# Performance work log

Hardware: AMD Instinct MI355X
Metric: run time of the kernel (lower is better)

## Reference

```python
import jax, jax.numpy as jnp
import numpy as np

N = 50000
E = 800000
FEAT = 512
HID = 256
CLS = 40
EPS = 1e-5


def setup_inputs() -> dict:
    key = jax.random.key(0)
    ks = jax.random.split(key, 8)
    x = jax.random.normal(ks[0], (N, FEAT), dtype=jnp.float32)
    edge_index = jax.random.randint(ks[1], (2, E), 0, N, dtype=jnp.int64)
    s = 0.05
    return {
        "x": x,
        "edge_index": edge_index,
        "W1": jax.random.normal(ks[2], (FEAT, HID), dtype=jnp.float32) * s,
        "b1": jnp.zeros((HID,), jnp.float32),
        "W2": jax.random.normal(ks[3], (HID, HID), dtype=jnp.float32) * s,
        "b2": jnp.zeros((HID,), jnp.float32),
        "W3": jax.random.normal(ks[4], (HID, CLS), dtype=jnp.float32) * s,
        "b3": jnp.zeros((CLS,), jnp.float32),
        "gamma": jnp.ones((HID,), jnp.float32),
        "beta": jnp.zeros((HID,), jnp.float32),
        "run_mean": jnp.zeros((HID,), jnp.float32),
        "run_var": jnp.ones((HID,), jnp.float32),
    }


def _edge_norm(edge_index):
    # add self-loops, then symmetric normalization D^-1/2 (A+I) D^-1/2
    loop = jnp.arange(N, dtype=edge_index.dtype)
    src = jnp.concatenate([edge_index[0], loop])
    dst = jnp.concatenate([edge_index[1], loop])
    deg = jax.ops.segment_sum(jnp.ones_like(dst, jnp.float32), dst, num_segments=N)
    inv_sqrt = jnp.where(deg > 0, jax.lax.rsqrt(jnp.maximum(deg, 1.0)), 0.0)
    norm = inv_sqrt[src] * inv_sqrt[dst]  # [E+N]
    return src, dst, norm


def _gcn_conv(x, W, b, src, dst, norm):
    h = x @ W                               # [N, out]
    msg = h[src] * norm[:, None]            # gather + scale, [E+N, out]
    out = jax.ops.segment_sum(msg, dst, num_segments=N)
    return out + b


def _bn_relu(x, gamma, beta, mean, var):
    return jax.nn.relu((x - mean) * jax.lax.rsqrt(var + EPS) * gamma + beta)


def reference(x, edge_index, W1, b1, W2, b2, W3, b3, gamma, beta, run_mean, run_var):
    src, dst, norm = _edge_norm(edge_index)
    h = _gcn_conv(x, W1, b1, src, dst, norm)
    h = _bn_relu(h, gamma, beta, run_mean, run_var)
    h = _gcn_conv(h, W2, b2, src, dst, norm)
    h = _bn_relu(h, gamma, beta, run_mean, run_var)
    h = _gcn_conv(h, W3, b3, src, dst, norm)
    return h
```

## Files before the change

kernel.cpp:

```cpp
#include <hip/hip_runtime.h>
#include <cstdint>
#include <cstddef>

#define FEAT 512
#define HID 256
#define CLS 40
#define EPS 1e-5f

typedef __attribute__((ext_vector_type(8))) short short8;
typedef __attribute__((ext_vector_type(4))) float f32x4v;


__device__ __forceinline__ unsigned short f2bf(float f) {
    union { float f; unsigned u; } v; v.f = f;
    unsigned r = v.u + 0x7FFF + ((v.u >> 16) & 1);
    return (unsigned short)(r >> 16);
}
__device__ __forceinline__ float bf2f(unsigned short h) {
    union { unsigned u; float f; } v; v.u = ((unsigned)h) << 16;
    return v.f;
}

typedef const __attribute__((address_space(1))) unsigned int* gas_ptr;
typedef __attribute__((address_space(3))) unsigned int* las_ptr;
__device__ __forceinline__ void lds_load16(const void* g, void* l) {
    __builtin_amdgcn_global_load_lds((gas_ptr)g, (las_ptr)l, 16, 0, 0);
}

__device__ __forceinline__ float4 f4add(float4 a, float4 b) {
    return make_float4(a.x + b.x, a.y + b.y, a.z + b.z, a.w + b.w);
}

__device__ __forceinline__ void accum_bf4(float4& a, ushort4 v) {
    a.x += bf2f(v.x); a.y += bf2f(v.y); a.z += bf2f(v.z); a.w += bf2f(v.w);
}


__global__ __launch_bounds__(256) void prep_cvt_kernel(
        const float* __restrict__ x, const float* __restrict__ W1, const float* __restrict__ W2,
        int* __restrict__ counts, int* __restrict__ fillpos,
        unsigned short* __restrict__ w1hi, unsigned short* __restrict__ w1lo,
        unsigned short* __restrict__ w2hi, unsigned short* __restrict__ w2lo,
        unsigned short* __restrict__ xbf, int N) {
    int i = blockIdx.x * 256 + threadIdx.x;
    const int n0 = N;
    const int n1 = FEAT * HID;
    const int n2 = HID * HID;
    const int n3 = N * FEAT / 8;
    if (i < n0) { counts[i] = 0; fillpos[i] = 0; return; }
    i -= n0;
    if (i < n1) {
        int k = i / HID, n = i % HID;
        float f = W1[i];
        unsigned short h = f2bf(f);
        w1hi[(size_t)n * FEAT + k] = h;
        w1lo[(size_t)n * FEAT + k] = f2bf(f - bf2f(h));
        return;
    }
    i -= n1;
    if (i < n2) {
        int k = i / HID, n = i % HID;
        float f = W2[i];
        unsigned short h = f2bf(f);
        w2hi[(size_t)n * HID + k] = h;
        w2lo[(size_t)n * HID + k] = f2bf(f - bf2f(h));
        return;
    }
    i -= n2;
    if (i < n3) {
        const float4* xp = (const float4*)x;
        float4 a = xp[2 * i], b = xp[2 * i + 1];
        float f[8] = {a.x, a.y, a.z, a.w, b.x, b.y, b.z, b.w};
        short8 h;
#pragma unroll
        for (int j = 0; j < 8; ++j) h[j] = (short)f2bf(f[j]);
        ((short8*)xbf)[i] = h;
    }
}


__global__ void hist_kernel(const int* __restrict__ dst, int* __restrict__ counts, int E) {
    int e = blockIdx.x * 256 + threadIdx.x;
    if (e < E) atomicAdd(&counts[dst[e]], 1);
}

__global__ void scan_block_kernel(const int* __restrict__ counts, int* __restrict__ row_ptr,
                                  int* __restrict__ blocksums, int n) {
    __shared__ int s[256];
    int tid = threadIdx.x;
    int i = blockIdx.x * 256 + tid;
    int v = (i < n) ? counts[i] : 0;
    s[tid] = v; __syncthreads();
    for (int off = 1; off < 256; off <<= 1) {
        int t = (tid >= off) ? s[tid - off] : 0;
        __syncthreads();
        s[tid] += t;
        __syncthreads();
    }
    if (i < n) row_ptr[i] = s[tid] - v;
    if (tid == 255) blocksums[blockIdx.x] = s[255];
}

__global__ void finalize_rowptr_kernel(int* __restrict__ row_ptr, const int* __restrict__ blocksums,
                                       const int* __restrict__ counts, float* __restrict__ inv_sqrt,
                                       int n, int E, int nb) {
    __shared__ int s[256];
    __shared__ int excl[256];
    int tid = threadIdx.x;
    int v = (tid < nb) ? blocksums[tid] : 0;
    s[tid] = v; __syncthreads();
    for (int off = 1; off < 256; off <<= 1) {
        int t = (tid >= off) ? s[tid - off] : 0;
        __syncthreads();
        s[tid] += t;
        __syncthreads();
    }
    excl[tid] = s[tid] - v;
    __syncthreads();
    int i = blockIdx.x * 256 + tid;
    if (i < n) {
        row_ptr[i] += excl[i >> 8];
        inv_sqrt[i] = rsqrtf((float)(counts[i] + 1));
    }
    if (i == 0) row_ptr[n] = E;
}

__global__ void fill_kernel(const int* __restrict__ src, const int* __restrict__ dst,
                            const int* __restrict__ row_ptr, int* __restrict__ fillpos,
                            int* __restrict__ src_sorted, int E) {
    int e = blockIdx.x * 256 + threadIdx.x;
    if (e < E) {
        int d = dst[e];
        int pos = row_ptr[d] + atomicAdd(&fillpos[d], 1);
        src_sorted[pos] = src[e];
    }
}


template<int BK>
__global__ __launch_bounds__(256) void gemm_mfma_kernel(
        const unsigned short* __restrict__ gA,
        const unsigned short* __restrict__ Wthi, const unsigned short* __restrict__ Wtlo,
        const float* __restrict__ inv_sqrt, unsigned short* __restrict__ C,
        int M, int K, int Ncol) {
    constexpr int BLK = 16 * BK;
    constexpr int CH = BK / 32;
    __shared__ unsigned short AhiL[2][128 * BK];
    __shared__ unsigned short BhiL[2][128 * BK];
    __shared__ unsigned short BloL[2][128 * BK];
    const int tid  = threadIdx.x;
    const int lane = tid & 63;
    const int w    = tid >> 6;
    const int wr   = w >> 1, wc = w & 1;
    const int lm   = lane & 15;
    const int lk8  = (lane >> 4) * 8;
    const int bm   = blockIdx.x * 128;
    const int bn   = blockIdx.y * 128;

    f32x4v acc[4][4] = {};

    int nc0 = bn + 16 * (2 * w) + lm;
    int nc1 = bn + 16 * (2 * w + 1) + lm;
    const unsigned short* gB_h0 = Wthi + (size_t)nc0 * K + lk8;
    const unsigned short* gB_h1 = Wthi + (size_t)nc1 * K + lk8;
    const unsigned short* gB_l0 = Wtlo + (size_t)nc0 * K + lk8;
    const unsigned short* gB_l1 = Wtlo + (size_t)nc1 * K + lk8;

    int ar0 = bm + 16 * (2 * w) + lm;     if (ar0 >= M) ar0 = M - 1;
    int ar1 = bm + 16 * (2 * w + 1) + lm; if (ar1 >= M) ar1 = M - 1;
    const unsigned short* gA_h0 = gA + (size_t)ar0 * K + lk8;
    const unsigned short* gA_h1 = gA + (size_t)ar1 * K + lk8;

    auto stage = [&](int buf, int k0) {
#pragma unroll
        for (int kk = 0; kk < CH; ++kk) {
            const int kg = k0 + 32 * kk;
            const int lo = kk * 512;
            lds_load16(gA_h0 + kg, &AhiL[buf][(2 * w) * BLK + lo]);
            lds_load16(gA_h1 + kg, &AhiL[buf][(2 * w + 1) * BLK + lo]);
            lds_load16(gB_h0 + kg, &BhiL[buf][(2 * w) * BLK + lo]);
            lds_load16(gB_h1 + kg, &BhiL[buf][(2 * w + 1) * BLK + lo]);
            lds_load16(gB_l0 + kg, &BloL[buf][(2 * w) * BLK + lo]);
            lds_load16(gB_l1 + kg, &BloL[buf][(2 * w + 1) * BLK + lo]);
        }
    };

    auto compute = [&](int buf) {
#pragma unroll
        for (int half = 0; half < CH; ++half) {
            const int ho = half * 512;
            short8 ah[4], bh[4], bv[4];
#pragma unroll
            for (int i = 0; i < 4; ++i) {
                int ao = (wr * 4 + i) * BLK + ho + lane * 8;
                int bo = (wc * 4 + i) * BLK + ho + lane * 8;
                ah[i] = *(const short8*)&AhiL[buf][ao];
                bh[i] = *(const short8*)&BhiL[buf][bo];
                bv[i] = *(const short8*)&BloL[buf][bo];
            }
#pragma unroll
            for (int i = 0; i < 4; ++i)
#pragma unroll
                for (int j = 0; j < 4; ++j) {
                    acc[i][j] = __builtin_amdgcn_mfma_f32_16x16x32_bf16(ah[i], bh[j], acc[i][j], 0, 0, 0);
                    acc[i][j] = __builtin_amdgcn_mfma_f32_16x16x32_bf16(ah[i], bv[j], acc[i][j], 0, 0, 0);
                }
        }
    };

    stage(0, 0);
    __syncthreads();
    int cur = 0;
    for (int k0 = BK; k0 < K; k0 += BK) {
        stage(cur ^ 1, k0);
        compute(cur);
        __syncthreads();
        cur ^= 1;
    }
    compute(cur);

    const int orow_base = bm + wr * 64;
    const int ocol_base = bn + wc * 64 + lm;
    const int rq = (lane >> 4) * 4;
#pragma unroll
    for (int i = 0; i < 4; ++i) {
#pragma unroll
        for (int r = 0; r < 4; ++r) {
            int row = orow_base + i * 16 + rq + r;
            if (row >= M) continue;
            float s = inv_sqrt[row];
            size_t rb = (size_t)row * Ncol;
#pragma unroll
            for (int j = 0; j < 4; ++j)
                C[rb + ocol_base + j * 16] = f2bf(acc[i][j][r] * s);
        }
    }
}


__global__ __launch_bounds__(256) void gemm_scaled_hl_kernel(
        const unsigned short* __restrict__ Ahi, const unsigned short* __restrict__ Alo,
        const float* __restrict__ W,
        const float* __restrict__ inv_sqrt, float* __restrict__ C,
        int M, int K, int Ncol) {
    __shared__ float As[16][64];
    __shared__ float Ws[16][64];
    int tid = threadIdx.x;
    int tm = tid >> 4;
    int tn = tid & 15;
    int bm = blockIdx.x * 64;
    int bn = blockIdx.y * 64;

    float acc[4][4] = {};

    int lr = tid >> 2;
    int lc = (tid & 3) << 2;
    int wr = tid >> 4;
    int wc = (tid & 15) << 2;
    int arow = bm + lr;
    bool aok = arow < M;
    bool wok = (bn + wc) < Ncol;
    const unsigned short* AhiRow = Ahi + (size_t)arow * K + lc;
    const unsigned short* AloRow = Alo + (size_t)arow * K + lc;

    for (int k0 = 0; k0 < K; k0 += 16) {
        float4 av = make_float4(0.f, 0.f, 0.f, 0.f);
        if (aok) {
            ushort4 hv = *(const ushort4*)(AhiRow + k0);
            ushort4 lv = *(const ushort4*)(AloRow + k0);
            av.x = bf2f(hv.x) + bf2f(lv.x);
            av.y = bf2f(hv.y) + bf2f(lv.y);
            av.z = bf2f(hv.z) + bf2f(lv.z);
            av.w = bf2f(hv.w) + bf2f(lv.w);
        }
        As[lc + 0][lr] = av.x; As[lc + 1][lr] = av.y;
        As[lc + 2][lr] = av.z; As[lc + 3][lr] = av.w;

        float4 wv = make_float4(0.f, 0.f, 0.f, 0.f);
        if (wok) wv = *(const float4*)(W + (size_t)(k0 + wr) * Ncol + bn + wc);
        *(float4*)&Ws[wr][wc] = wv;
        __syncthreads();

#pragma unroll
        for (int k = 0; k < 16; ++k) {
            const float4 a4 = *(const float4*)&As[k][tm << 2];
            const float4 b4 = *(const float4*)&Ws[k][tn << 2];
            float a[4] = {a4.x, a4.y, a4.z, a4.w};
            float b[4] = {b4.x, b4.y, b4.z, b4.w};
#pragma unroll
            for (int i = 0; i < 4; ++i)
#pragma unroll
                for (int j = 0; j < 4; ++j)
                    acc[i][j] = fmaf(a[i], b[j], acc[i][j]);
        }
        __syncthreads();
    }

#pragma unroll
    for (int i = 0; i < 4; ++i) {
        int row = bm + (tm << 2) + i;
        if (row >= M) continue;
        float s = inv_sqrt[row];
        int col = bn + (tn << 2);
        if (col < Ncol) {
            float4 o = make_float4(acc[i][0] * s, acc[i][1] * s, acc[i][2] * s, acc[i][3] * s);
            *(float4*)&C[(size_t)row * Ncol + col] = o;
        }
    }
}


template<bool WRITE_LO>
__global__ __launch_bounds__(256) void agg_bn_hl_kernel(
        const unsigned short* __restrict__ g, const int* __restrict__ row_ptr,
        const int* __restrict__ srcs, const float* __restrict__ inv_sqrt,
        const float* __restrict__ bias, const float* __restrict__ gamma,
        const float* __restrict__ beta, const float* __restrict__ mean,
        const float* __restrict__ var,
        unsigned short* __restrict__ out_hi, unsigned short* __restrict__ out_lo, int n) {
    int node = (blockIdx.x << 2) + (threadIdx.x >> 6);
    int lane = threadIdx.x & 63;
    if (node >= n) return;
    const ushort4* gp = (const ushort4*)g;
    float4 acc0 = make_float4(0.f, 0.f, 0.f, 0.f);
    float4 acc1 = make_float4(0.f, 0.f, 0.f, 0.f);
    accum_bf4(acc0, gp[(size_t)node * 64 + lane]);
    int beg = row_ptr[node];
    int cnt = row_ptr[node + 1] - beg;

    for (int base = 0; base < cnt; base += 64) {
        int m = cnt - base; if (m > 64) m = 64;
        int idx = (lane < m) ? srcs[beg + base + lane] : 0;
        int j = 0;
        for (; j + 8 <= m; j += 8) {
            int s0 = __shfl(idx, j + 0), s1 = __shfl(idx, j + 1);
            int s2 = __shfl(idx, j + 2), s3 = __shfl(idx, j + 3);
            int s4 = __shfl(idx, j + 4), s5 = __shfl(idx, j + 5);
            int s6 = __shfl(idx, j + 6), s7 = __shfl(idx, j + 7);
            ushort4 v0 = gp[(size_t)s0 * 64 + lane];
            ushort4 v1 = gp[(size_t)s1 * 64 + lane];
            ushort4 v2 = gp[(size_t)s2 * 64 + lane];
            ushort4 v3 = gp[(size_t)s3 * 64 + lane];
            ushort4 v4 = gp[(size_t)s4 * 64 + lane];
            ushort4 v5 = gp[(size_t)s5 * 64 + lane];
            ushort4 v6 = gp[(size_t)s6 * 64 + lane];
            ushort4 v7 = gp[(size_t)s7 * 64 + lane];
            accum_bf4(acc0, v0); accum_bf4(acc0, v1);
            accum_bf4(acc0, v2); accum_bf4(acc0, v3);
            accum_bf4(acc1, v4); accum_bf4(acc1, v5);
            accum_bf4(acc1, v6); accum_bf4(acc1, v7);
        }
        for (; j < m; ++j) {
            int s = __shfl(idx, j);
            accum_bf4(acc0, gp[(size_t)s * 64 + lane]);
        }
    }
    float4 acc = f4add(acc0, acc1);

    float inv = inv_sqrt[node];
    float4 b4  = ((const float4*)bias)[lane];
    float4 ga4 = ((const float4*)gamma)[lane];
    float4 be4 = ((const float4*)beta)[lane];
    float4 m4  = ((const float4*)mean)[lane];
    float4 v4  = ((const float4*)var)[lane];
    float4 o;
    o.x = fmaxf((acc.x * inv + b4.x - m4.x) * (ga4.x * rsqrtf(v4.x + EPS)) + be4.x, 0.f);
    o.y = fmaxf((acc.y * inv + b4.y - m4.y) * (ga4.y * rsqrtf(v4.y + EPS)) + be4.y, 0.f);
    o.z = fmaxf((acc.z * inv + b4.z - m4.z) * (ga4.z * rsqrtf(v4.z + EPS)) + be4.z, 0.f);
    o.w = fmaxf((acc.w * inv + b4.w - m4.w) * (ga4.w * rsqrtf(v4.w + EPS)) + be4.w, 0.f);
    ushort4 oh;
    oh.x = f2bf(o.x); oh.y = f2bf(o.y); oh.z = f2bf(o.z); oh.w = f2bf(o.w);
    ((ushort4*)out_hi)[(size_t)node * 64 + lane] = oh;
    if (WRITE_LO) {
        ushort4 ol;
        ol.x = f2bf(o.x - bf2f(oh.x));
        ol.y = f2bf(o.y - bf2f(oh.y));
        ol.z = f2bf(o.z - bf2f(oh.z));
        ol.w = f2bf(o.w - bf2f(oh.w));
        ((ushort4*)out_lo)[(size_t)node * 64 + lane] = ol;
    }
}


__global__ __launch_bounds__(256) void agg_final_kernel(
        const float* __restrict__ g, const int* __restrict__ row_ptr,
        const int* __restrict__ srcs, const float* __restrict__ inv_sqrt,
        const float* __restrict__ bias, float* __restrict__ out, int n) {
    int node = (blockIdx.x << 2) + (threadIdx.x >> 6);
    int lane = threadIdx.x & 63;
    if (node >= n) return;
    int flane = (lane < CLS) ? lane : 0;
    float acc0 = g[(size_t)node * CLS + flane];
    float acc1 = 0.f;
    int beg = row_ptr[node];
    int cnt = row_ptr[node + 1] - beg;

    for (int base = 0; base < cnt; base += 64) {
        int m = cnt - base; if (m > 64) m = 64;
        int idx = (lane < m) ? srcs[beg + base + lane] : 0;
        int j = 0;
        for (; j + 8 <= m; j += 8) {
            int s0 = __shfl(idx, j + 0), s1 = __shfl(idx, j + 1);
            int s2 = __shfl(idx, j + 2), s3 = __shfl(idx, j + 3);
            int s4 = __shfl(idx, j + 4), s5 = __shfl(idx, j + 5);
            int s6 = __shfl(idx, j + 6), s7 = __shfl(idx, j + 7);
            float v0 = g[(size_t)s0 * CLS + flane];
            float v1 = g[(size_t)s1 * CLS + flane];
            float v2 = g[(size_t)s2 * CLS + flane];
            float v3 = g[(size_t)s3 * CLS + flane];
            float v4 = g[(size_t)s4 * CLS + flane];
            float v5 = g[(size_t)s5 * CLS + flane];
            float v6 = g[(size_t)s6 * CLS + flane];
            float v7 = g[(size_t)s7 * CLS + flane];
            acc0 += (v0 + v1) + (v2 + v3);
            acc1 += (v4 + v5) + (v6 + v7);
        }
        for (; j < m; ++j) {
            int s = __shfl(idx, j);
            acc0 += g[(size_t)s * CLS + flane];
        }
    }
    if (lane < CLS)
        out[(size_t)node * CLS + lane] = (acc0 + acc1) * inv_sqrt[node] + bias[lane];
}


extern "C" void kernel_launch(void* const* d_in, const int* in_sizes, int n_in,
                              void* d_out, int out_size, void* d_ws, size_t ws_size,
                              hipStream_t stream) {
    const float* x     = (const float*)d_in[0];
    const int*   edges = (const int*)d_in[1];
    const float* W1    = (const float*)d_in[2];
    const float* b1    = (const float*)d_in[3];
    const float* W2    = (const float*)d_in[4];
    const float* b2    = (const float*)d_in[5];
    const float* W3    = (const float*)d_in[6];
    const float* b3    = (const float*)d_in[7];
    const float* gamma = (const float*)d_in[8];
    const float* beta  = (const float*)d_in[9];
    const float* mean  = (const float*)d_in[10];
    const float* var   = (const float*)d_in[11];

    const int N = in_sizes[0] / FEAT;
    const int E = in_sizes[1] / 2;
    const int* src = edges;
    const int* dst = edges + E;

    char* ws = (char*)d_ws;
    auto alloc = [&](size_t bytes) -> char* {
        char* p = ws;
        ws += (bytes + 255) & ~(size_t)255;
        return p;
    };
    int*   counts     = (int*)  alloc((size_t)N * 4);
    int*   fillpos    = (int*)  alloc((size_t)N * 4);
    int*   row_ptr    = (int*)  alloc((size_t)(N + 1) * 4);
    int*   blocksums  = (int*)  alloc(256 * 4);
    float* inv_sqrt   = (float*)alloc((size_t)N * 4);
    int*   src_sorted = (int*)  alloc((size_t)E * 4);
    unsigned short* w1hi = (unsigned short*)alloc((size_t)FEAT * HID * 2);
    unsigned short* w1lo = (unsigned short*)alloc((size_t)FEAT * HID * 2);
    unsigned short* w2hi = (unsigned short*)alloc((size_t)HID * HID * 2);
    unsigned short* w2lo = (unsigned short*)alloc((size_t)HID * HID * 2);
    unsigned short* g    = (unsigned short*)alloc((size_t)N * HID * 2);
    unsigned short* h_hi = (unsigned short*)alloc((size_t)N * HID * 2);
    unsigned short* h_lo = (unsigned short*)alloc((size_t)N * HID * 2);
    unsigned short* xbf  = h_hi;

    int nb = (N + 255) / 256;
    int eb = (E + 255) / 256;

    int prep_items = N + FEAT * HID + HID * HID + N * FEAT / 8;
    prep_cvt_kernel<<<(prep_items + 255) / 256, 256, 0, stream>>>(
        x, W1, W2, counts, fillpos, w1hi, w1lo, w2hi, w2lo, xbf, N);
    hist_kernel<<<eb, 256, 0, stream>>>(dst, counts, E);
    scan_block_kernel<<<nb, 256, 0, stream>>>(counts, row_ptr, blocksums, N);
    finalize_rowptr_kernel<<<nb, 256, 0, stream>>>(row_ptr, blocksums, counts, inv_sqrt, N, E, nb);
    fill_kernel<<<eb, 256, 0, stream>>>(src, dst, row_ptr, fillpos, src_sorted, E);

    dim3 mfma_grid((N + 127) / 128, HID / 128);
    dim3 gemm3_grid((N + 63) / 64, 1);
    dim3 agg_grid((N + 3) / 4);

    gemm_mfma_kernel<32><<<mfma_grid, 256, 0, stream>>>(
        xbf, w1hi, w1lo, inv_sqrt, g, N, FEAT, HID);
    agg_bn_hl_kernel<false><<<agg_grid, 256, 0, stream>>>(g, row_ptr, src_sorted, inv_sqrt,
                                                          b1, gamma, beta, mean, var, h_hi, nullptr, N);
    gemm_mfma_kernel<32><<<mfma_grid, 256, 0, stream>>>(
        h_hi, w2hi, w2lo, inv_sqrt, g, N, HID, HID);
    agg_bn_hl_kernel<true><<<agg_grid, 256, 0, stream>>>(g, row_ptr, src_sorted, inv_sqrt,
                                                         b2, gamma, beta, mean, var, h_hi, h_lo, N);
    float* g3 = (float*)g;
    gemm_scaled_hl_kernel<<<gemm3_grid, 256, 0, stream>>>(h_hi, h_lo, W3, inv_sqrt, g3, N, HID, CLS);
    agg_final_kernel<<<agg_grid, 256, 0, stream>>>(g3, row_ptr, src_sorted, inv_sqrt,
                                                   b3, (float*)d_out, N);
}
```

Measured before the change: 548.1 us.

## Load GEMM MFMA fragments directly from global into registers, bypassing LDS

Replaces the LDS double-buffered global_load_lds staging in the MFMA GEMM with direct per-lane global loads into register fragments. A register double buffer is software-pipelined over a compile-time K loop. This removes LDS traffic and block barriers. In exchange, A and B fragments are no longer shared across waves through LDS, so each wave issues redundant global and L2 loads, and register pressure rises.

```diff
diff --git a/kernel.cpp b/kernel.cpp
--- a/kernel.cpp
+++ b/kernel.cpp
@@ -19,12 +19,6 @@
 __device__ __forceinline__ float bf2f(unsigned short h) {
     union { unsigned u; float f; } v; v.u = ((unsigned)h) << 16;
     return v.f;
-}
-
-typedef const __attribute__((address_space(1))) unsigned int* gas_ptr;
-typedef __attribute__((address_space(3))) unsigned int* las_ptr;
-__device__ __forceinline__ void lds_load16(const void* g, void* l) {
-    __builtin_amdgcn_global_load_lds((gas_ptr)g, (las_ptr)l, 16, 0, 0);
 }
 
 __device__ __forceinline__ float4 f4add(float4 a, float4 b) {
@@ -137,17 +131,29 @@
 }
 
 
-template<int BK>
-__global__ __launch_bounds__(256) void gemm_mfma_kernel(
+#define LOADF(A, B, V, k0)                                    \
+    _Pragma("unroll")                                         \
+    for (int i = 0; i < 4; ++i) {                             \
+        A[i] = *(const short8*)(pa[i] + (k0));                \
+        B[i] = *(const short8*)(pbh[i] + (k0));               \
+        V[i] = *(const short8*)(pbv[i] + (k0));               \
+    }
+
+#define COMPF(A, B, V)                                        \
+    _Pragma("unroll")                                         \
+    for (int i = 0; i < 4; ++i)                               \
+        _Pragma("unroll")                                     \
+        for (int j = 0; j < 4; ++j) {                         \
+            acc[i][j] = __builtin_amdgcn_mfma_f32_16x16x32_bf16(A[i], B[j], acc[i][j], 0, 0, 0); \
+            acc[i][j] = __builtin_amdgcn_mfma_f32_16x16x32_bf16(A[i], V[j], acc[i][j], 0, 0, 0); \
+        }
+
+template<int K>
+__global__ __launch_bounds__(256) void gemm_mfma_direct_kernel(
         const unsigned short* __restrict__ gA,
         const unsigned short* __restrict__ Wthi, const unsigned short* __restrict__ Wtlo,
         const float* __restrict__ inv_sqrt, unsigned short* __restrict__ C,
-        int M, int K, int Ncol) {
-    constexpr int BLK = 16 * BK;
-    constexpr int CH = BK / 32;
-    __shared__ unsigned short AhiL[2][128 * BK];
-    __shared__ unsigned short BhiL[2][128 * BK];
-    __shared__ unsigned short BloL[2][128 * BK];
+        int M, int Ncol) {
     const int tid  = threadIdx.x;
     const int lane = tid & 63;
     const int w    = tid >> 6;
@@ -159,65 +165,32 @@
 
     f32x4v acc[4][4] = {};
 
-    int nc0 = bn + 16 * (2 * w) + lm;
-    int nc1 = bn + 16 * (2 * w + 1) + lm;
-    const unsigned short* gB_h0 = Wthi + (size_t)nc0 * K + lk8;
-    const unsigned short* gB_h1 = Wthi + (size_t)nc1 * K + lk8;
-    const unsigned short* gB_l0 = Wtlo + (size_t)nc0 * K + lk8;
-    const unsigned short* gB_l1 = Wtlo + (size_t)nc1 * K + lk8;
-
-    int ar0 = bm + 16 * (2 * w) + lm;     if (ar0 >= M) ar0 = M - 1;
-    int ar1 = bm + 16 * (2 * w + 1) + lm; if (ar1 >= M) ar1 = M - 1;
-    const unsigned short* gA_h0 = gA + (size_t)ar0 * K + lk8;
-    const unsigned short* gA_h1 = gA + (size_t)ar1 * K + lk8;
-
-    auto stage = [&](int buf, int k0) {
-#pragma unroll
-        for (int kk = 0; kk < CH; ++kk) {
-            const int kg = k0 + 32 * kk;
-            const int lo = kk * 512;
-            lds_load16(gA_h0 + kg, &AhiL[buf][(2 * w) * BLK + lo]);
-            lds_load16(gA_h1 + kg, &AhiL[buf][(2 * w + 1) * BLK + lo]);
-            lds_load16(gB_h0 + kg, &BhiL[buf][(2 * w) * BLK + lo]);
-            lds_load16(gB_h1 + kg, &BhiL[buf][(2 * w + 1) * BLK + lo]);
-            lds_load16(gB_l0 + kg, &BloL[buf][(2 * w) * BLK + lo]);
-            lds_load16(gB_l1 + kg, &BloL[buf][(2 * w + 1) * BLK + lo]);
-        }
-    };
-
-    auto compute = [&](int buf) {
-#pragma unroll
-        for (int half = 0; half < CH; ++half) {
-            const int ho = half * 512;
-            short8 ah[4], bh[4], bv[4];
-#pragma unroll
-            for (int i = 0; i < 4; ++i) {
-                int ao = (wr * 4 + i) * BLK + ho + lane * 8;
-                int bo = (wc * 4 + i) * BLK + ho + lane * 8;
-                ah[i] = *(const short8*)&AhiL[buf][ao];
-                bh[i] = *(const short8*)&BhiL[buf][bo];
-                bv[i] = *(const short8*)&BloL[buf][bo];
-            }
-#pragma unroll
-            for (int i = 0; i < 4; ++i)
-#pragma unroll
-                for (int j = 0; j < 4; ++j) {
-                    acc[i][j] = __builtin_amdgcn_mfma_f32_16x16x32_bf16(ah[i], bh[j], acc[i][j], 0, 0, 0);
-                    acc[i][j] = __builtin_amdgcn_mfma_f32_16x16x32_bf16(ah[i], bv[j], acc[i][j], 0, 0, 0);
-                }
-        }
-    };
-
-    stage(0, 0);
-    __syncthreads();
-    int cur = 0;
-    for (int k0 = BK; k0 < K; k0 += BK) {
-        stage(cur ^ 1, k0);
-        compute(cur);
-        __syncthreads();
-        cur ^= 1;
-    }
-    compute(cur);
+    const unsigned short* pa[4];
+    const unsigned short* pbh[4];
+    const unsigned short* pbv[4];
+#pragma unroll
+    for (int i = 0; i < 4; ++i) {
+        int ar = bm + wr * 64 + i * 16 + lm; if (ar >= M) ar = M - 1;
+        pa[i]  = gA   + (size_t)ar * K + lk8;
+        int nc = bn + wc * 64 + i * 16 + lm;
+        pbh[i] = Wthi + (size_t)nc * K + lk8;
+        pbv[i] = Wtlo + (size_t)nc * K + lk8;
+    }
+
+    short8 a0[4], b0[4], v0[4], a1[4], b1[4], v1[4];
+
+    LOADF(a0, b0, v0, 0);
+    int k0 = 0;
+#pragma unroll
+    for (; k0 + 64 < K; k0 += 64) {
+        LOADF(a1, b1, v1, k0 + 32);
+        COMPF(a0, b0, v0);
+        LOADF(a0, b0, v0, k0 + 64);
+        COMPF(a1, b1, v1);
+    }
+    LOADF(a1, b1, v1, K - 32);
+    COMPF(a0, b0, v0);
+    COMPF(a1, b1, v1);
 
     const int orow_base = bm + wr * 64;
     const int ocol_base = bn + wc * 64 + lm;
@@ -482,12 +455,12 @@
     dim3 gemm3_grid((N + 63) / 64, 1);
     dim3 agg_grid((N + 3) / 4);
 
-    gemm_mfma_kernel<32><<<mfma_grid, 256, 0, stream>>>(
-        xbf, w1hi, w1lo, inv_sqrt, g, N, FEAT, HID);
+    gemm_mfma_direct_kernel<FEAT><<<mfma_grid, 256, 0, stream>>>(
+        xbf, w1hi, w1lo, inv_sqrt, g, N, HID);
     agg_bn_hl_kernel<false><<<agg_grid, 256, 0, stream>>>(g, row_ptr, src_sorted, inv_sqrt,
                                                           b1, gamma, beta, mean, var, h_hi, nullptr, N);
-    gemm_mfma_kernel<32><<<mfma_grid, 256, 0, stream>>>(
-        h_hi, w2hi, w2lo, inv_sqrt, g, N, HID, HID);
+    gemm_mfma_direct_kernel<HID><<<mfma_grid, 256, 0, stream>>>(
+        h_hi, w2hi, w2lo, inv_sqrt, g, N, HID);
     agg_bn_hl_kernel<true><<<agg_grid, 256, 0, stream>>>(g, row_ptr, src_sorted, inv_sqrt,
                                                          b2, gamma, beta, mean, var, h_hi, h_lo, N);
     float* g3 = (float*)g;
```

New measurement: 595.3 us. 1.09x slower.

## Use 512-thread full-width MFMA GEMM with triple-buffered async LDS pipeline

Applied to the files above, without the earlier changes.

Replaces the 256-thread, 128x128-tile MFMA GEMM with a 512-thread kernel where each block covers 128 rows and all 256 output columns. The A tile is loaded once per block instead of once per column half. K is a compile-time template parameter and the loop is fully unrolled. Global-to-LDS copies are triple-buffered and paced with explicit vmcnt waits and raw s_barrier calls, so loads run ahead of compute. The cost is more LDS per block, half as many blocks, and hand-tuned wait counts that must stay in step with the number of loads per stage.

```diff
diff --git a/kernel.cpp b/kernel.cpp
--- a/kernel.cpp
+++ b/kernel.cpp
@@ -137,90 +137,84 @@
 }
 
 
-template<int BK>
-__global__ __launch_bounds__(256) void gemm_mfma_kernel(
+template<int K>
+__global__ __launch_bounds__(512) void gemm_mfma_pipe_kernel(
         const unsigned short* __restrict__ gA,
         const unsigned short* __restrict__ Wthi, const unsigned short* __restrict__ Wtlo,
         const float* __restrict__ inv_sqrt, unsigned short* __restrict__ C,
-        int M, int K, int Ncol) {
-    constexpr int BLK = 16 * BK;
-    constexpr int CH = BK / 32;
-    __shared__ unsigned short AhiL[2][128 * BK];
-    __shared__ unsigned short BhiL[2][128 * BK];
-    __shared__ unsigned short BloL[2][128 * BK];
+        int M) {
+    constexpr int NT = K / 32;
+    __shared__ unsigned short Abuf [3][8  * 512];
+    __shared__ unsigned short Bhbuf[3][16 * 512];
+    __shared__ unsigned short Blbuf[3][16 * 512];
     const int tid  = threadIdx.x;
     const int lane = tid & 63;
     const int w    = tid >> 6;
-    const int wr   = w >> 1, wc = w & 1;
+    const int wr   = w >> 2, wc = w & 3;
     const int lm   = lane & 15;
     const int lk8  = (lane >> 4) * 8;
     const int bm   = blockIdx.x * 128;
-    const int bn   = blockIdx.y * 128;
 
     f32x4v acc[4][4] = {};
 
-    int nc0 = bn + 16 * (2 * w) + lm;
-    int nc1 = bn + 16 * (2 * w + 1) + lm;
-    const unsigned short* gB_h0 = Wthi + (size_t)nc0 * K + lk8;
-    const unsigned short* gB_h1 = Wthi + (size_t)nc1 * K + lk8;
-    const unsigned short* gB_l0 = Wtlo + (size_t)nc0 * K + lk8;
-    const unsigned short* gB_l1 = Wtlo + (size_t)nc1 * K + lk8;
-
-    int ar0 = bm + 16 * (2 * w) + lm;     if (ar0 >= M) ar0 = M - 1;
-    int ar1 = bm + 16 * (2 * w + 1) + lm; if (ar1 >= M) ar1 = M - 1;
-    const unsigned short* gA_h0 = gA + (size_t)ar0 * K + lk8;
-    const unsigned short* gA_h1 = gA + (size_t)ar1 * K + lk8;
-
-    auto stage = [&](int buf, int k0) {
-#pragma unroll
-        for (int kk = 0; kk < CH; ++kk) {
-            const int kg = k0 + 32 * kk;
-            const int lo = kk * 512;
-            lds_load16(gA_h0 + kg, &AhiL[buf][(2 * w) * BLK + lo]);
-            lds_load16(gA_h1 + kg, &AhiL[buf][(2 * w + 1) * BLK + lo]);
-            lds_load16(gB_h0 + kg, &BhiL[buf][(2 * w) * BLK + lo]);
-            lds_load16(gB_h1 + kg, &BhiL[buf][(2 * w + 1) * BLK + lo]);
-            lds_load16(gB_l0 + kg, &BloL[buf][(2 * w) * BLK + lo]);
-            lds_load16(gB_l1 + kg, &BloL[buf][(2 * w + 1) * BLK + lo]);
-        }
+    int ar = bm + 16 * w + lm; if (ar >= M) ar = M - 1;
+    const unsigned short* gA_w = gA   + (size_t)ar * K + lk8;
+    const unsigned short* gBh0 = Wthi + (size_t)(16 * (2 * w)     + lm) * K + lk8;
+    const unsigned short* gBh1 = Wthi + (size_t)(16 * (2 * w + 1) + lm) * K + lk8;
+    const unsigned short* gBl0 = Wtlo + (size_t)(16 * (2 * w)     + lm) * K + lk8;
+    const unsigned short* gBl1 = Wtlo + (size_t)(16 * (2 * w + 1) + lm) * K + lk8;
+
+    auto stage = [&](int buf, int t) {
+        const int kg = t * 32;
+        lds_load16(gA_w + kg, &Abuf [buf][w * 512]);
+        lds_load16(gBh0 + kg, &Bhbuf[buf][(2 * w) * 512]);
+        lds_load16(gBh1 + kg, &Bhbuf[buf][(2 * w + 1) * 512]);
+        lds_load16(gBl0 + kg, &Blbuf[buf][(2 * w) * 512]);
+        lds_load16(gBl1 + kg, &Blbuf[buf][(2 * w + 1) * 512]);
     };
 
     auto compute = [&](int buf) {
-#pragma unroll
-        for (int half = 0; half < CH; ++half) {
-            const int ho = half * 512;
-            short8 ah[4], bh[4], bv[4];
-#pragma unroll
-            for (int i = 0; i < 4; ++i) {
-                int ao = (wr * 4 + i) * BLK + ho + lane * 8;
-                int bo = (wc * 4 + i) * BLK + ho + lane * 8;
-                ah[i] = *(const short8*)&AhiL[buf][ao];
-                bh[i] = *(const short8*)&BhiL[buf][bo];
-                bv[i] = *(const short8*)&BloL[buf][bo];
+        short8 ah[4], bh[4], bv[4];
+#pragma unroll
+        for (int i = 0; i < 4; ++i) {
+            ah[i] = *(const short8*)&Abuf [buf][(wr * 4 + i) * 512 + lane * 8];
+            bh[i] = *(const short8*)&Bhbuf[buf][(wc * 4 + i) * 512 + lane * 8];
+            bv[i] = *(const short8*)&Blbuf[buf][(wc * 4 + i) * 512 + lane * 8];
+        }
+#pragma unroll
+        for (int i = 0; i < 4; ++i)
+#pragma unroll
+            for (int j = 0; j < 4; ++j) {
+                acc[i][j] = __builtin_amdgcn_mfma_f32_16x16x32_bf16(ah[i], bh[j], acc[i][j], 0, 0, 0);
+                acc[i][j] = __builtin_amdgcn_mfma_f32_16x16x32_bf16(ah[i], bv[j], acc[i][j], 0, 0, 0);
             }
-#pragma unroll
-            for (int i = 0; i < 4; ++i)
-#pragma unroll
-                for (int j = 0; j < 4; ++j) {
-                    acc[i][j] = __builtin_amdgcn_mfma_f32_16x16x32_bf16(ah[i], bh[j], acc[i][j], 0, 0, 0);
-                    acc[i][j] = __builtin_amdgcn_mfma_f32_16x16x32_bf16(ah[i], bv[j], acc[i][j], 0, 0, 0);
-                }
-        }
     };
 
-    stage(0, 0);
-    __syncthreads();
-    int cur = 0;
-    for (int k0 = BK; k0 < K; k0 += BK) {
-        stage(cur ^ 1, k0);
-        compute(cur);
-        __syncthreads();
-        cur ^= 1;
-    }
-    compute(cur);
+    stage(0, 0); stage(1, 1); stage(2, 2);
+    asm volatile("s_waitcnt vmcnt(10)" ::: "memory");
+    __builtin_amdgcn_s_barrier();
+    __builtin_amdgcn_sched_barrier(0);
+
+#pragma unroll
+    for (int t = 0; t < NT; ++t) {
+        const int buf = t % 3;
+        compute(buf);
+        __builtin_amdgcn_s_barrier();
+        __builtin_amdgcn_sched_barrier(0);
+        if (t + 3 < NT) {
+            stage(buf, t + 3);
+            asm volatile("s_waitcnt vmcnt(10)" ::: "memory");
+        } else if (t + 2 < NT) {
+            asm volatile("s_waitcnt vmcnt(5)" ::: "memory");
+        } else if (t + 1 < NT) {
+            asm volatile("s_waitcnt vmcnt(0)" ::: "memory");
+        }
+        __builtin_amdgcn_s_barrier();
+        __builtin_amdgcn_sched_barrier(0);
+    }
 
     const int orow_base = bm + wr * 64;
-    const int ocol_base = bn + wc * 64 + lm;
+    const int ocol_base = wc * 64 + lm;
     const int rq = (lane >> 4) * 4;
 #pragma unroll
     for (int i = 0; i < 4; ++i) {
@@ -229,7 +223,7 @@
             int row = orow_base + i * 16 + rq + r;
             if (row >= M) continue;
             float s = inv_sqrt[row];
-            size_t rb = (size_t)row * Ncol;
+            size_t rb = (size_t)row * HID;
 #pragma unroll
             for (int j = 0; j < 4; ++j)
                 C[rb + ocol_base + j * 16] = f2bf(acc[i][j][r] * s);
@@ -478,16 +472,16 @@
     finalize_rowptr_kernel<<<nb, 256, 0, stream>>>(row_ptr, blocksums, counts, inv_sqrt, N, E, nb);
     fill_kernel<<<eb, 256, 0, stream>>>(src, dst, row_ptr, fillpos, src_sorted, E);
 
-    dim3 mfma_grid((N + 127) / 128, HID / 128);
+    dim3 pipe_grid((N + 127) / 128);
     dim3 gemm3_grid((N + 63) / 64, 1);
     dim3 agg_grid((N + 3) / 4);
 
-    gemm_mfma_kernel<32><<<mfma_grid, 256, 0, stream>>>(
-        xbf, w1hi, w1lo, inv_sqrt, g, N, FEAT, HID);
+    gemm_mfma_pipe_kernel<FEAT><<<pipe_grid, 512, 0, stream>>>(
+        xbf, w1hi, w1lo, inv_sqrt, g, N);
     agg_bn_hl_kernel<false><<<agg_grid, 256, 0, stream>>>(g, row_ptr, src_sorted, inv_sqrt,
                                                           b1, gamma, beta, mean, var, h_hi, nullptr, N);
-    gemm_mfma_kernel<32><<<mfma_grid, 256, 0, stream>>>(
-        h_hi, w2hi, w2lo, inv_sqrt, g, N, HID, HID);
+    gemm_mfma_pipe_kernel<HID><<<pipe_grid, 512, 0, stream>>>(
+        h_hi, w2hi, w2lo, inv_sqrt, g, N);
     agg_bn_hl_kernel<true><<<agg_grid, 256, 0, stream>>>(g, row_ptr, src_sorted, inv_sqrt,
                                                          b2, gamma, beta, mean, var, h_hi, h_lo, N);
     float* g3 = (float*)g;
```

After: 539.5 us. No clear change (-1.6%).
